# Optimization experiments

Measured on AMD Instinct MI355X. Metric: run time of the kernel, lower is better.

## Reference

```python
import math
import jax, jax.numpy as jnp
import numpy as np

E_DIM = 256
R_DIM = 256
HID = 512
B = 1024
H = 200
LN_EPS = 1e-5


def layer_norm(x, g, b):
    mu = jnp.mean(x, axis=-1, keepdims=True)
    var = jnp.mean((x - mu) ** 2, axis=-1, keepdims=True)
    return (x - mu) * jax.lax.rsqrt(var + LN_EPS) * g + b


def setup_inputs() -> dict:
    key = jax.random.key(0)
    ks = jax.random.split(key, 16)
    s = lambda fan: 1.0 / math.sqrt(fan)
    inp = {
        "e_emb": jax.random.normal(ks[0], (B, E_DIM), jnp.float32),
        "hist_ent_emb": jax.random.normal(ks[1], (B, H, E_DIM), jnp.float32),
        "hist_rel_emb": jax.random.normal(ks[2], (B, H, R_DIM), jnp.float32),
        "hist_time_raw": jax.random.randint(ks[3], (B, H), 0, 1000, jnp.int32),
        "query_time": jax.random.randint(ks[4], (B,), 0, 1000, jnp.int32),
        "hist_mask": jax.random.bernoulli(ks[5], 0.8, (B, H)),
        # parameters
        "W_rel": jax.random.uniform(ks[6], (E_DIM, R_DIM), jnp.float32, -s(R_DIM), s(R_DIM)),
        "W_q": jax.random.uniform(ks[7], (E_DIM, E_DIM), jnp.float32, -s(E_DIM), s(E_DIM)),
        "log_gamma": jnp.asarray(-3.0, jnp.float32),
        "W1": jax.random.uniform(ks[8], (2 * E_DIM, 4 * E_DIM), jnp.float32, -s(4 * E_DIM), s(4 * E_DIM)),
        "b1": jnp.zeros((2 * E_DIM,), jnp.float32),
        "ln1_g": jnp.ones((2 * E_DIM,), jnp.float32),
        "ln1_b": jnp.zeros((2 * E_DIM,), jnp.float32),
        "W2": jax.random.uniform(ks[9], (E_DIM, 2 * E_DIM), jnp.float32, -s(2 * E_DIM), s(2 * E_DIM)),
        "b2": jnp.zeros((E_DIM,), jnp.float32),
        "ln2_g": jnp.ones((E_DIM,), jnp.float32),
        "ln2_b": jnp.zeros((E_DIM,), jnp.float32),
        "Wc": jax.random.uniform(ks[10], (HID, E_DIM), jnp.float32, -s(E_DIM), s(E_DIM)),
        "bc": jnp.zeros((HID,), jnp.float32),
        "lnc_g": jnp.ones((HID,), jnp.float32),
        "lnc_b": jnp.zeros((HID,), jnp.float32),
    }
    return inp


def reference(e_emb, hist_ent_emb, hist_rel_emb, hist_time_raw, query_time, hist_mask,
              W_rel, W_q, log_gamma, W1, b1, ln1_g, ln1_b, W2, b2, ln2_g, ln2_b,
              Wc, bc, lnc_g, lnc_b):
    E = e_emb.shape[-1]
    # DistMult messages: (B,H,E)
    rel_projected = jnp.einsum("bhr,er->bhe", hist_rel_emb, W_rel)
    messages = hist_ent_emb * rel_projected
    # time decay
    time_diff = jnp.maximum(query_time.astype(jnp.float32)[:, None] - hist_time_raw.astype(jnp.float32), 0.0)
    decay = jnp.exp(-jnp.exp(log_gamma) * time_diff)  # (B,H)
    messages_dec = messages * decay[..., None]
    # query-conditioned attention
    q_repr = e_emb @ W_q.T  # (B,E)
    attn_raw = jnp.einsum("be,bhe->bh", q_repr, messages_dec) / math.sqrt(E)
    attn_raw = jnp.where(hist_mask, attn_raw, -1e9)
    attn = jax.nn.softmax(attn_raw, axis=-1)
    # PNA aggregation over valid neighbors
    valid_f = hist_mask.astype(jnp.float32)[..., None]  # (B,H,1)
    n_valid = jnp.maximum(jnp.sum(valid_f, axis=1), 1.0)  # (B,1)
    valid_msgs = messages * valid_f
    mean_msg = jnp.sum(valid_msgs, axis=1) / n_valid
    max_msg = jnp.max(valid_msgs, axis=1)
    attn_msg = jnp.einsum("bh,bhe->be", attn, messages)
    combined = jnp.concatenate([mean_msg, max_msg, attn_msg, e_emb], axis=-1)  # (B,4E)
    # out_proj MLP (dropout = identity, eval mode)
    h1 = jax.nn.gelu(layer_norm(combined @ W1.T + b1, ln1_g, ln1_b), approximate=False)
    dynamic_emb = layer_norm(h1 @ W2.T + b2, ln2_g, ln2_b)  # (B,E)
    ctx = jax.nn.gelu(layer_norm(dynamic_emb @ Wc.T + bc, lnc_g, lnc_b), approximate=False)  # (B,HID)
    return dynamic_emb, ctx
```

## Files before the change

### kernel.cpp

```cpp
#include <hip/hip_runtime.h>
#include <hip/hip_bf16.h>
#include <math.h>

#define B_SZ 1024
#define H_SZ 200
#define E_SZ 256
#define R_SZ 256
#define LN_EPS 1e-5f
#define NEG_HUGE -3.0e38f

typedef short bf16x8 __attribute__((ext_vector_type(8)));
typedef float f32x4 __attribute__((ext_vector_type(4)));

static __device__ inline short f2bf(float f) {
  union { float f; unsigned int u; } v; v.f = f;
  unsigned int u = v.u;
  unsigned int r = (u + 0x7fffu + ((u >> 16) & 1u)) >> 16;
  return (short)(unsigned short)r;
}

static __device__ inline float mask_at(const void* m, size_t idx, int is_b8) {
  if (is_b8) return ((const unsigned char*)m)[idx] ? 1.f : 0.f;
  return ((const int*)m)[idx] ? 1.f : 0.f;
}

__global__ void detect_mask_kernel(const unsigned char* __restrict__ mask,
                                   int* __restrict__ flag) {
  __shared__ int cnt;
  if (threadIdx.x == 0) cnt = 0;
  __syncthreads();
  int c = 0;
  for (int i = threadIdx.x; i < 4096; i += 256) c += mask[i] ? 1 : 0;
  atomicAdd(&cnt, c);
  __syncthreads();
  if (threadIdx.x == 0) *flag = (cnt > 2048) ? 1 : 0;
}

__global__ __launch_bounds__(256) void qrepr_kernel(
    const float* __restrict__ e_emb, const float* __restrict__ Wq,
    float* __restrict__ q_out) {
  __shared__ float emb[4][E_SZ];
  const int t = threadIdx.x;
  const int b0 = blockIdx.x * 4;
  for (int r = 0; r < 4; ++r) emb[r][t] = e_emb[(size_t)(b0 + r) * E_SZ + t];
  __syncthreads();
  float acc[4] = {0.f, 0.f, 0.f, 0.f};
  const float4* wrow = (const float4*)(Wq + (size_t)t * E_SZ);
  for (int k4 = 0; k4 < E_SZ / 4; ++k4) {
    float4 w = wrow[k4];
    const int k = k4 * 4;
#pragma unroll
    for (int r = 0; r < 4; ++r)
      acc[r] += emb[r][k] * w.x + emb[r][k + 1] * w.y + emb[r][k + 2] * w.z +
                emb[r][k + 3] * w.w;
  }
  for (int r = 0; r < 4; ++r) q_out[(size_t)(b0 + r) * E_SZ + t] = acc[r];
}

#define AGG_LDS_BYTES 152576

__global__ __launch_bounds__(512, 2) void agg_kernel(
    const float* __restrict__ rel, const float* __restrict__ ent,
    const int* __restrict__ htime, const int* __restrict__ qtime,
    const void* __restrict__ mask, const int* __restrict__ mflag,
    const float* __restrict__ Wrel, const float* __restrict__ qws,
    const float* __restrict__ e_emb, const float* __restrict__ log_gamma,
    float* __restrict__ comb) {
  extern __shared__ char smem[];
  short* Wsw = (short*)smem;
  short* Asw = (short*)(smem + 131072);
  float* q_s = (float*)(smem + 147456);
  float* attn_acc = (float*)(smem + 148480);
  float* mean_b = (float*)(smem + 149504);
  float* max_b = (float*)(smem + 150528);
  float* s_part = (float*)(smem + 151552);
  float* decay_s = (float*)(smem + 152064);
  float* maskf_s = (float*)(smem + 152192);
  float* p_s = (float*)(smem + 152320);
  float* scal = (float*)(smem + 152448);

  const int t = threadIdx.x;
  const int lane = t & 63;
  const int w = t >> 6;
  const int rh = w >> 2;
  const int cg = w & 3;
  const int q4 = lane >> 4;
  const int cl = lane & 15;
  const float gamma = expf(log_gamma[0]);
  const int is_b8 = *mflag;

  for (int pass = 0; pass < 16; ++pass) {
    const int idx = pass * 512 + t;
    const int e = idx >> 5;
    const int rc = idx & 31;
    const float4* src = (const float4*)(Wrel + (size_t)e * R_SZ + rc * 8);
    float4 a0 = src[0], a1 = src[1];
    const int ks = rc >> 2;
    const int lidx = ((rc & 3) << 4) | (e & 15);
    const int csub = e >> 4;
    bf16x8 v;
    v[0] = f2bf(a0.x); v[1] = f2bf(a0.y); v[2] = f2bf(a0.z); v[3] = f2bf(a0.w);
    v[4] = f2bf(a1.x); v[5] = f2bf(a1.y); v[6] = f2bf(a1.z); v[7] = f2bf(a1.w);
    *(bf16x8*)(Wsw + (((csub * 8 + ks) * 64 + lidx) << 3)) = v;
  }

  for (int bi = 0; bi < 4; ++bi) {
    const int b = blockIdx.x + 256 * bi;
    if (t < 256) { attn_acc[t] = 0.f; q_s[t] = qws[(size_t)b * E_SZ + t]; }
    if (t == 0) { scal[0] = NEG_HUGE; scal[1] = 0.f; scal[2] = 0.f; scal[3] = 0.f; }
    float mean4[4] = {0.f, 0.f, 0.f, 0.f};
    float max4[4] = {NEG_HUGE, NEG_HUGE, NEG_HUGE, NEG_HUGE};
    const int qt = qtime[b];
    __syncthreads();

    for (int tile = 0; tile < 7; ++tile) {
      const int h0 = tile * 32;
      {
        const int row = t >> 4;
        const int rcc = t & 15;
        const int h = h0 + row;
        bf16x8 v0 = {}; bf16x8 v1 = {};
        if (h < H_SZ) {
          const float4* src =
              (const float4*)(rel + ((size_t)b * H_SZ + h) * R_SZ + rcc * 16);
          float4 a0 = src[0], a1 = src[1], a2 = src[2], a3 = src[3];
          v0[0] = f2bf(a0.x); v0[1] = f2bf(a0.y); v0[2] = f2bf(a0.z); v0[3] = f2bf(a0.w);
          v0[4] = f2bf(a1.x); v0[5] = f2bf(a1.y); v0[6] = f2bf(a1.z); v0[7] = f2bf(a1.w);
          v1[0] = f2bf(a2.x); v1[1] = f2bf(a2.y); v1[2] = f2bf(a2.z); v1[3] = f2bf(a2.w);
          v1[4] = f2bf(a3.x); v1[5] = f2bf(a3.y); v1[6] = f2bf(a3.z); v1[7] = f2bf(a3.w);
        }
        const int rh2 = row >> 4, rlow = row & 15;
        const int rr0 = rcc * 2, rr1 = rcc * 2 + 1;
        *(bf16x8*)(Asw + (((rh2 * 8 + (rr0 >> 2)) * 64 + (((rr0 & 3) << 4) | rlow)) << 3)) = v0;
        *(bf16x8*)(Asw + (((rh2 * 8 + (rr1 >> 2)) * 64 + (((rr1 & 3) << 4) | rlow)) << 3)) = v1;
      }
      if (t < 32) {
        const int h = h0 + t;
        float mf = 0.f, dc = 0.f;
        if (h < H_SZ) {
          mf = mask_at(mask, (size_t)b * H_SZ + h, is_b8);
          float td = fmaxf((float)(qt - htime[(size_t)b * H_SZ + h]), 0.f);
          dc = expf(-gamma * td);
        }
        maskf_s[t] = mf; decay_s[t] = dc;
      }
      __syncthreads();

      f32x4 acc[4] = {};
      for (int ks = 0; ks < 8; ++ks) {
        bf16x8 av = *(bf16x8*)(Asw + (((rh * 8 + ks) * 64 + lane) << 3));
#pragma unroll
        for (int sub = 0; sub < 4; ++sub) {
          bf16x8 bv = *(bf16x8*)(Wsw + ((((cg * 4 + sub) * 8 + ks) * 64 + lane) << 3));
          acc[sub] = __builtin_amdgcn_mfma_f32_16x16x32_bf16(av, bv, acc[sub], 0, 0, 0);
        }
      }

      float msgv[16];
      float sc[4];
#pragma unroll
      for (int reg = 0; reg < 4; ++reg) {
        const int row = rh * 16 + q4 * 4 + reg;
        const int h = h0 + row;
        const float mf = maskf_s[row];
        const bool realrow = (h < H_SZ);
        float srow = 0.f;
#pragma unroll
        for (int sub = 0; sub < 4; ++sub) {
          const int e = cg * 64 + sub * 16 + cl;
          float entv = realrow ? ent[((size_t)b * H_SZ + h) * E_SZ + e] : 0.f;
          float m = acc[sub][reg] * entv;
          msgv[reg * 4 + sub] = m;
          mean4[sub] += mf * m;
          float cand = realrow ? (mf != 0.f ? m : 0.f) : NEG_HUGE;
          max4[sub] = fmaxf(max4[sub], cand);
          srow += q_s[e] * m;
        }
        sc[reg] = srow;
      }
#pragma unroll
      for (int m = 1; m <= 8; m <<= 1)
#pragma unroll
        for (int reg = 0; reg < 4; ++reg) sc[reg] += __shfl_xor(sc[reg], m, 64);
      if (cl == 0)
#pragma unroll
        for (int reg = 0; reg < 4; ++reg)
          s_part[(rh * 16 + q4 * 4 + reg) * 4 + cg] = sc[reg];
      __syncthreads();

      if (w == 0) {
        const int row = lane & 31;
        const int h = h0 + row;
        float srow = s_part[row * 4] + s_part[row * 4 + 1] +
                     s_part[row * 4 + 2] + s_part[row * 4 + 3];
        float s;
        if (h >= H_SZ) s = NEG_HUGE;
        else if (maskf_s[row] == 0.f) s = -1e9f;
        else s = decay_s[row] * srow * 0.0625f;
        float mt = s;
#pragma unroll
        for (int m = 1; m <= 16; m <<= 1) mt = fmaxf(mt, __shfl_xor(mt, m, 64));
        const float m_old = scal[0];
        const float m_new = fmaxf(m_old, mt);
        const float alpha = expf(m_old - m_new);
        const float p = expf(s - m_new);
        float lt = p;
#pragma unroll
        for (int m = 1; m <= 16; m <<= 1) lt += __shfl_xor(lt, m, 64);
        if (lane == 0) {
          scal[0] = m_new;
          scal[1] = scal[1] * alpha + lt;
          scal[2] = alpha;
        }
        if (lane < 32) p_s[row] = p;
      }
      __syncthreads();
      {
        const float alpha = scal[2];
        if (t < 256) attn_acc[t] *= alpha;
      }
      __syncthreads();
      float av4[4];
#pragma unroll
      for (int sub = 0; sub < 4; ++sub) {
        float v = 0.f;
#pragma unroll
        for (int reg = 0; reg < 4; ++reg)
          v += p_s[rh * 16 + q4 * 4 + reg] * msgv[reg * 4 + sub];
        v += __shfl_xor(v, 16, 64);
        v += __shfl_xor(v, 32, 64);
        av4[sub] = v;
      }
      if (q4 == 0)
#pragma unroll
        for (int sub = 0; sub < 4; ++sub)
          atomicAdd(&attn_acc[cg * 64 + sub * 16 + cl], av4[sub]);
      __syncthreads();
    }

#pragma unroll
    for (int sub = 0; sub < 4; ++sub) {
      float mv = mean4[sub];
      mv += __shfl_xor(mv, 16, 64); mv += __shfl_xor(mv, 32, 64);
      float xv = max4[sub];
      xv = fmaxf(xv, __shfl_xor(xv, 16, 64));
      xv = fmaxf(xv, __shfl_xor(xv, 32, 64));
      mean4[sub] = mv; max4[sub] = xv;
    }
    if (rh == 0 && q4 == 0) {
#pragma unroll
      for (int sub = 0; sub < 4; ++sub) {
        mean_b[cg * 64 + sub * 16 + cl] = mean4[sub];
        max_b[cg * 64 + sub * 16 + cl] = max4[sub];
      }
    }
    if (t < H_SZ) atomicAdd(&scal[3], mask_at(mask, (size_t)b * H_SZ + t, is_b8));
    __syncthreads();
    if (rh == 1 && q4 == 0) {
#pragma unroll
      for (int sub = 0; sub < 4; ++sub) {
        const int e = cg * 64 + sub * 16 + cl;
        mean_b[e] += mean4[sub];
        max_b[e] = fmaxf(max_b[e], max4[sub]);
      }
    }
    __syncthreads();
    if (t < 256) {
      const float nv = fmaxf(scal[3], 1.f);
      const float l = scal[1];
      float* dst = comb + (size_t)b * 1024;
      dst[t] = mean_b[t] / nv;
      dst[256 + t] = max_b[t];
      dst[512 + t] = attn_acc[t] / l;
      dst[768 + t] = e_emb[(size_t)b * E_SZ + t];
    }
    __syncthreads();
  }
}

template <int K, int N, bool GELU>
__global__ __launch_bounds__(256) void mlp_kernel(
    const float* __restrict__ X, const float* __restrict__ W,
    const float* __restrict__ bias, const float* __restrict__ lng,
    const float* __restrict__ lnb, float* __restrict__ Y) {
  constexpr int CPT = N / 256;
  __shared__ float xs[4][K];
  __shared__ float pre[4][N];
  __shared__ float red[4][2];
  const int t = threadIdx.x;
  const size_t b0 = (size_t)blockIdx.x * 4;
  for (int r = 0; r < 4; ++r)
    for (int k = t; k < K; k += 256) xs[r][k] = X[(b0 + r) * K + k];
  __syncthreads();
  float acc[4][CPT];
#pragma unroll
  for (int r = 0; r < 4; ++r)
#pragma unroll
    for (int c = 0; c < CPT; ++c) acc[r][c] = 0.f;
  for (int ci = 0; ci < CPT; ++ci) {
    const int c = t + 256 * ci;
    const float4* wr = (const float4*)(W + (size_t)c * K);
    for (int k4 = 0; k4 < K / 4; ++k4) {
      float4 wv = wr[k4];
      const int k = k4 * 4;
#pragma unroll
      for (int r = 0; r < 4; ++r)
        acc[r][ci] += xs[r][k] * wv.x + xs[r][k + 1] * wv.y +
                      xs[r][k + 2] * wv.z + xs[r][k + 3] * wv.w;
    }
  }
  for (int ci = 0; ci < CPT; ++ci) {
    const int c = t + 256 * ci;
#pragma unroll
    for (int r = 0; r < 4; ++r) pre[r][c] = acc[r][ci] + bias[c];
  }
  __syncthreads();
  if (t < 64) {
    const int r = t >> 4, ch = t & 15;
    float s = 0.f, s2 = 0.f;
    for (int i = ch * (N / 16); i < (ch + 1) * (N / 16); ++i) {
      float v = pre[r][i]; s += v; s2 += v * v;
    }
#pragma unroll
    for (int m = 1; m <= 8; m <<= 1) {
      s += __shfl_xor(s, m, 64);
      s2 += __shfl_xor(s2, m, 64);
    }
    if (ch == 0) { red[r][0] = s / N; red[r][1] = s2 / N; }
  }
  __syncthreads();
  for (int ci = 0; ci < CPT; ++ci) {
    const int c = t + 256 * ci;
#pragma unroll
    for (int r = 0; r < 4; ++r) {
      const float mu = red[r][0];
      const float var = fmaxf(red[r][1] - mu * mu, 0.f);
      float x = (pre[r][c] - mu) * rsqrtf(var + LN_EPS) * lng[c] + lnb[c];
      if (GELU) x = 0.5f * x * (1.f + erff(x * 0.70710678118654752f));
      Y[(b0 + r) * N + c] = x;
    }
  }
}

extern "C" void kernel_launch(void* const* d_in, const int* in_sizes, int n_in,
                              void* d_out, int out_size, void* d_ws,
                              size_t ws_size, hipStream_t stream) {
  const float* e_emb = (const float*)d_in[0];
  const float* ent = (const float*)d_in[1];
  const float* rel = (const float*)d_in[2];
  const int* ht = (const int*)d_in[3];
  const int* qt = (const int*)d_in[4];
  const void* mask = d_in[5];
  const float* Wrel = (const float*)d_in[6];
  const float* Wq = (const float*)d_in[7];
  const float* lg = (const float*)d_in[8];
  const float* W1 = (const float*)d_in[9];
  const float* b1 = (const float*)d_in[10];
  const float* ln1g = (const float*)d_in[11];
  const float* ln1b = (const float*)d_in[12];
  const float* W2 = (const float*)d_in[13];
  const float* b2 = (const float*)d_in[14];
  const float* ln2g = (const float*)d_in[15];
  const float* ln2b = (const float*)d_in[16];
  const float* Wc = (const float*)d_in[17];
  const float* bc = (const float*)d_in[18];
  const float* lncg = (const float*)d_in[19];
  const float* lncb = (const float*)d_in[20];

  float* q_ws = (float*)d_ws;
  float* comb = (float*)((char*)d_ws + (1 << 20));
  float* t1 = (float*)((char*)d_ws + (5 << 20));
  int* mflag = (int*)((char*)d_ws + (7 << 20));
  float* dyn = (float*)d_out;
  float* ctx = (float*)d_out + (size_t)B_SZ * E_SZ;

  (void)hipFuncSetAttribute((const void*)agg_kernel,
                            hipFuncAttributeMaxDynamicSharedMemorySize,
                            AGG_LDS_BYTES);

  detect_mask_kernel<<<1, 256, 0, stream>>>((const unsigned char*)mask, mflag);
  qrepr_kernel<<<256, 256, 0, stream>>>(e_emb, Wq, q_ws);
  agg_kernel<<<256, 512, AGG_LDS_BYTES, stream>>>(rel, ent, ht, qt, mask, mflag,
                                                  Wrel, q_ws, e_emb, lg, comb);
  mlp_kernel<1024, 512, true><<<256, 256, 0, stream>>>(comb, W1, b1, ln1g, ln1b, t1);
  mlp_kernel<512, 256, false><<<256, 256, 0, stream>>>(t1, W2, b2, ln2g, ln2b, dyn);
  mlp_kernel<256, 512, true><<<256, 256, 0, stream>>>(dyn, Wc, bc, lncg, lncb, ctx);
}
```

Measured before the change: 673.5 us.

## Rewrite aggregation with prefetch pipelining, two-pass softmax, and MFMA MLP GEMMs

Several independent changes land together. W_rel is pre-swizzled to bf16 once in a separate kernel, and the aggregation kernel now prefetches the next tile's rel and ent rows into registers while computing the current one. It uses an XOR-swizzled LDS layout and replaces the per-tile online softmax (several barriers per tile) with one softmax pass over bf16 messages kept in registers. The scalar fp32 MLP and q-projection kernels become a tiled bf16 MFMA GEMM plus separate LayerNorm/GELU kernels. The aim is to cut barrier count and redundant global loads and to move the GEMMs onto matrix cores, at the cost of bf16 rounding in the messages and MLP inputs, more kernel launches, and higher register pressure.

```diff
diff --git a/kernel.cpp b/kernel.cpp
--- a/kernel.cpp
+++ b/kernel.cpp
@@ -12,14 +12,24 @@
 typedef short bf16x8 __attribute__((ext_vector_type(8)));
 typedef float f32x4 __attribute__((ext_vector_type(4)));
 
-static __device__ inline short f2bf(float f) {
-  union { float f; unsigned int u; } v; v.f = f;
-  unsigned int u = v.u;
-  unsigned int r = (u + 0x7fffu + ((u >> 16) & 1u)) >> 16;
+static __device__ __forceinline__ short f2bf(float f) {
+  union { float f; unsigned u; } v; v.f = f;
+  unsigned r = (v.u + 0x7fffu + ((v.u >> 16) & 1u)) >> 16;
   return (short)(unsigned short)r;
 }
-
-static __device__ inline float mask_at(const void* m, size_t idx, int is_b8) {
+static __device__ __forceinline__ float bf2f(unsigned short h) {
+  union { unsigned u; float f; } v; v.u = ((unsigned)h) << 16; return v.f;
+}
+static __device__ __forceinline__ int slotxor(int frame, int q4f, int mf, int ks) {
+  return frame * 64 + (q4f << 4) + ((mf ^ (ks & 3) ^ ((q4f & 3) << 2)) & 15);
+}
+static __device__ __forceinline__ bf16x8 pack8(const float4& a, const float4& b) {
+  bf16x8 v;
+  v[0] = f2bf(a.x); v[1] = f2bf(a.y); v[2] = f2bf(a.z); v[3] = f2bf(a.w);
+  v[4] = f2bf(b.x); v[5] = f2bf(b.y); v[6] = f2bf(b.z); v[7] = f2bf(b.w);
+  return v;
+}
+static __device__ __forceinline__ float mask_at(const void* m, size_t idx, int is_b8) {
   if (is_b8) return ((const unsigned char*)m)[idx] ? 1.f : 0.f;
   return ((const int*)m)[idx] ? 1.f : 0.f;
 }
@@ -36,238 +46,249 @@
   if (threadIdx.x == 0) *flag = (cnt > 2048) ? 1 : 0;
 }
 
-__global__ __launch_bounds__(256) void qrepr_kernel(
-    const float* __restrict__ e_emb, const float* __restrict__ Wq,
-    float* __restrict__ q_out) {
-  __shared__ float emb[4][E_SZ];
-  const int t = threadIdx.x;
-  const int b0 = blockIdx.x * 4;
-  for (int r = 0; r < 4; ++r) emb[r][t] = e_emb[(size_t)(b0 + r) * E_SZ + t];
-  __syncthreads();
-  float acc[4] = {0.f, 0.f, 0.f, 0.f};
-  const float4* wrow = (const float4*)(Wq + (size_t)t * E_SZ);
-  for (int k4 = 0; k4 < E_SZ / 4; ++k4) {
-    float4 w = wrow[k4];
-    const int k = k4 * 4;
-#pragma unroll
-    for (int r = 0; r < 4; ++r)
-      acc[r] += emb[r][k] * w.x + emb[r][k + 1] * w.y + emb[r][k + 2] * w.z +
-                emb[r][k + 3] * w.w;
-  }
-  for (int r = 0; r < 4; ++r) q_out[(size_t)(b0 + r) * E_SZ + t] = acc[r];
-}
-
-#define AGG_LDS_BYTES 152576
+__global__ __launch_bounds__(256) void prep_wrel_kernel(
+    const float* __restrict__ Wrel, short* __restrict__ Wg) {
+  const int s = blockIdx.x * 256 + threadIdx.x;
+  const int frame = s >> 6, lf = s & 63, q4f = lf >> 4, mfx = lf & 15;
+  const int ks = frame & 7, csub = frame >> 3;
+  const int m = (mfx ^ (ks & 3) ^ ((q4f & 3) << 2)) & 15;
+  const int e = csub * 16 + m;
+  const int r0 = ks * 32 + q4f * 8;
+  const float4* src = (const float4*)(Wrel + (size_t)e * R_SZ + r0);
+  float4 a = src[0], b = src[1];
+  *(bf16x8*)(Wg + (size_t)s * 8) = pack8(a, b);
+}
+
+#define AGG_LDS_BYTES 157200
 
 __global__ __launch_bounds__(512, 2) void agg_kernel(
     const float* __restrict__ rel, const float* __restrict__ ent,
     const int* __restrict__ htime, const int* __restrict__ qtime,
     const void* __restrict__ mask, const int* __restrict__ mflag,
-    const float* __restrict__ Wrel, const float* __restrict__ qws,
+    const short* __restrict__ Wg, const float* __restrict__ qws,
     const float* __restrict__ e_emb, const float* __restrict__ log_gamma,
     float* __restrict__ comb) {
   extern __shared__ char smem[];
   short* Wsw = (short*)smem;
   short* Asw = (short*)(smem + 131072);
-  float* q_s = (float*)(smem + 147456);
-  float* attn_acc = (float*)(smem + 148480);
-  float* mean_b = (float*)(smem + 149504);
-  float* max_b = (float*)(smem + 150528);
-  float* s_part = (float*)(smem + 151552);
-  float* decay_s = (float*)(smem + 152064);
-  float* maskf_s = (float*)(smem + 152192);
-  float* p_s = (float*)(smem + 152320);
-  float* scal = (float*)(smem + 152448);
-
-  const int t = threadIdx.x;
-  const int lane = t & 63;
-  const int w = t >> 6;
-  const int rh = w >> 2;
-  const int cg = w & 3;
-  const int q4 = lane >> 4;
-  const int cl = lane & 15;
+  float* maskf_s = (float*)(smem + 147456);
+  float* decay_s = (float*)(smem + 148480);
+  float* score_s = (float*)(smem + 149504);
+  float* s_part  = (float*)(smem + 150528);
+  float* attn_acc = (float*)(smem + 154112);
+  float* mean_b  = (float*)(smem + 155136);
+  float* max_b   = (float*)(smem + 156160);
+  float* scal    = (float*)(smem + 157184);
+
+  const int t = threadIdx.x, lane = t & 63, w = t >> 6;
+  const int rh = w >> 2, cg = w & 3, q4 = lane >> 4, cl = lane & 15;
   const float gamma = expf(log_gamma[0]);
   const int is_b8 = *mflag;
 
-  for (int pass = 0; pass < 16; ++pass) {
-    const int idx = pass * 512 + t;
-    const int e = idx >> 5;
-    const int rc = idx & 31;
-    const float4* src = (const float4*)(Wrel + (size_t)e * R_SZ + rc * 8);
-    float4 a0 = src[0], a1 = src[1];
-    const int ks = rc >> 2;
-    const int lidx = ((rc & 3) << 4) | (e & 15);
-    const int csub = e >> 4;
-    bf16x8 v;
-    v[0] = f2bf(a0.x); v[1] = f2bf(a0.y); v[2] = f2bf(a0.z); v[3] = f2bf(a0.w);
-    v[4] = f2bf(a1.x); v[5] = f2bf(a1.y); v[6] = f2bf(a1.z); v[7] = f2bf(a1.w);
-    *(bf16x8*)(Wsw + (((csub * 8 + ks) * 64 + lidx) << 3)) = v;
-  }
+  {
+    const bf16x8* src = (const bf16x8*)Wg;
+    bf16x8* dst = (bf16x8*)Wsw;
+#pragma unroll
+    for (int p = 0; p < 16; ++p) dst[p * 512 + t] = src[p * 512 + t];
+  }
+
+  const int arow = t >> 4, rcc = t & 15;
 
   for (int bi = 0; bi < 4; ++bi) {
     const int b = blockIdx.x + 256 * bi;
-    if (t < 256) { attn_acc[t] = 0.f; q_s[t] = qws[(size_t)b * E_SZ + t]; }
-    if (t == 0) { scal[0] = NEG_HUGE; scal[1] = 0.f; scal[2] = 0.f; scal[3] = 0.f; }
+    const int qt = qtime[b];
+    if (t < 256) {
+      attn_acc[t] = 0.f;
+      float mf = 0.f, dc = 0.f;
+      if (t < H_SZ) {
+        mf = mask_at(mask, (size_t)b * H_SZ + t, is_b8);
+        float td = fmaxf((float)(qt - htime[(size_t)b * H_SZ + t]), 0.f);
+        dc = expf(-gamma * td);
+      }
+      maskf_s[t] = mf; decay_s[t] = dc;
+    }
+    float qv[4];
+#pragma unroll
+    for (int sub = 0; sub < 4; ++sub)
+      qv[sub] = qws[(size_t)b * E_SZ + cg * 64 + sub * 16 + cl];
+
+    float4 c0, c1, c2, c3;
+    {
+      const int hc = min(arow, H_SZ - 1);
+      const float4* src = (const float4*)(rel + ((size_t)b * H_SZ + hc) * R_SZ + rcc * 16);
+      c0 = src[0]; c1 = src[1]; c2 = src[2]; c3 = src[3];
+    }
+    float entb[16];
+#pragma unroll
+    for (int reg = 0; reg < 4; ++reg) {
+      const int hc = min(rh * 16 + q4 * 4 + reg, H_SZ - 1);
+      const float* ep = ent + ((size_t)b * H_SZ + hc) * E_SZ + cg * 64 + cl;
+#pragma unroll
+      for (int sub = 0; sub < 4; ++sub) entb[reg * 4 + sub] = ep[sub * 16];
+    }
+    {
+      const int rb = arow >> 4, m = arow & 15;
+      bf16x8 v0 = pack8(c0, c1), v1 = pack8(c2, c3);
+      int k8 = rcc * 2, ks = k8 >> 2, qw = k8 & 3;
+      *(bf16x8*)(Asw + slotxor(rb * 8 + ks, qw, m, ks) * 8) = v0;
+      k8 = rcc * 2 + 1; ks = k8 >> 2; qw = k8 & 3;
+      *(bf16x8*)(Asw + slotxor(rb * 8 + ks, qw, m, ks) * 8) = v1;
+    }
+    __syncthreads();
+
     float mean4[4] = {0.f, 0.f, 0.f, 0.f};
     float max4[4] = {NEG_HUGE, NEG_HUGE, NEG_HUGE, NEG_HUGE};
-    const int qt = qtime[b];
-    __syncthreads();
-
+    unsigned msgp[56];
+
+#pragma unroll
     for (int tile = 0; tile < 7; ++tile) {
       const int h0 = tile * 32;
-      {
-        const int row = t >> 4;
-        const int rcc = t & 15;
-        const int h = h0 + row;
-        bf16x8 v0 = {}; bf16x8 v1 = {};
-        if (h < H_SZ) {
-          const float4* src =
-              (const float4*)(rel + ((size_t)b * H_SZ + h) * R_SZ + rcc * 16);
-          float4 a0 = src[0], a1 = src[1], a2 = src[2], a3 = src[3];
-          v0[0] = f2bf(a0.x); v0[1] = f2bf(a0.y); v0[2] = f2bf(a0.z); v0[3] = f2bf(a0.w);
-          v0[4] = f2bf(a1.x); v0[5] = f2bf(a1.y); v0[6] = f2bf(a1.z); v0[7] = f2bf(a1.w);
-          v1[0] = f2bf(a2.x); v1[1] = f2bf(a2.y); v1[2] = f2bf(a2.z); v1[3] = f2bf(a2.w);
-          v1[4] = f2bf(a3.x); v1[5] = f2bf(a3.y); v1[6] = f2bf(a3.z); v1[7] = f2bf(a3.w);
+      float4 n0, n1, n2, n3;
+      float entn[16];
+      if (tile < 6) {
+        const int hc = min(h0 + 32 + arow, H_SZ - 1);
+        const float4* src = (const float4*)(rel + ((size_t)b * H_SZ + hc) * R_SZ + rcc * 16);
+        n0 = src[0]; n1 = src[1]; n2 = src[2]; n3 = src[3];
+#pragma unroll
+        for (int reg = 0; reg < 4; ++reg) {
+          const int hc2 = min(h0 + 32 + rh * 16 + q4 * 4 + reg, H_SZ - 1);
+          const float* ep = ent + ((size_t)b * H_SZ + hc2) * E_SZ + cg * 64 + cl;
+#pragma unroll
+          for (int sub = 0; sub < 4; ++sub) entn[reg * 4 + sub] = ep[sub * 16];
         }
-        const int rh2 = row >> 4, rlow = row & 15;
-        const int rr0 = rcc * 2, rr1 = rcc * 2 + 1;
-        *(bf16x8*)(Asw + (((rh2 * 8 + (rr0 >> 2)) * 64 + (((rr0 & 3) << 4) | rlow)) << 3)) = v0;
-        *(bf16x8*)(Asw + (((rh2 * 8 + (rr1 >> 2)) * 64 + (((rr1 & 3) << 4) | rlow)) << 3)) = v1;
-      }
-      if (t < 32) {
-        const int h = h0 + t;
-        float mf = 0.f, dc = 0.f;
-        if (h < H_SZ) {
-          mf = mask_at(mask, (size_t)b * H_SZ + h, is_b8);
-          float td = fmaxf((float)(qt - htime[(size_t)b * H_SZ + h]), 0.f);
-          dc = expf(-gamma * td);
-        }
-        maskf_s[t] = mf; decay_s[t] = dc;
-      }
-      __syncthreads();
-
+      }
       f32x4 acc[4] = {};
+#pragma unroll
       for (int ks = 0; ks < 8; ++ks) {
-        bf16x8 av = *(bf16x8*)(Asw + (((rh * 8 + ks) * 64 + lane) << 3));
+        bf16x8 av = *(const bf16x8*)(Asw + slotxor(rh * 8 + ks, q4, cl, ks) * 8);
 #pragma unroll
         for (int sub = 0; sub < 4; ++sub) {
-          bf16x8 bv = *(bf16x8*)(Wsw + ((((cg * 4 + sub) * 8 + ks) * 64 + lane) << 3));
+          bf16x8 bv = *(const bf16x8*)(Wsw + slotxor((cg * 4 + sub) * 8 + ks, q4, cl, ks) * 8);
           acc[sub] = __builtin_amdgcn_mfma_f32_16x16x32_bf16(av, bv, acc[sub], 0, 0, 0);
         }
       }
-
-      float msgv[16];
       float sc[4];
 #pragma unroll
       for (int reg = 0; reg < 4; ++reg) {
         const int row = rh * 16 + q4 * 4 + reg;
-        const int h = h0 + row;
-        const float mf = maskf_s[row];
-        const bool realrow = (h < H_SZ);
-        float srow = 0.f;
+        const int hg = h0 + row;
+        const float mf = maskf_s[hg];
+        const bool rr = hg < H_SZ;
+        float srow = 0.f, mtmp[4];
 #pragma unroll
         for (int sub = 0; sub < 4; ++sub) {
-          const int e = cg * 64 + sub * 16 + cl;
-          float entv = realrow ? ent[((size_t)b * H_SZ + h) * E_SZ + e] : 0.f;
-          float m = acc[sub][reg] * entv;
-          msgv[reg * 4 + sub] = m;
+          float m = rr ? acc[sub][reg] * entb[reg * 4 + sub] : 0.f;
+          mtmp[sub] = m;
           mean4[sub] += mf * m;
-          float cand = realrow ? (mf != 0.f ? m : 0.f) : NEG_HUGE;
+          float cand = rr ? (mf != 0.f ? m : 0.f) : NEG_HUGE;
           max4[sub] = fmaxf(max4[sub], cand);
-          srow += q_s[e] * m;
+          srow += qv[sub] * m;
         }
         sc[reg] = srow;
-      }
-#pragma unroll
-      for (int m = 1; m <= 8; m <<= 1)
-#pragma unroll
-        for (int reg = 0; reg < 4; ++reg) sc[reg] += __shfl_xor(sc[reg], m, 64);
+        msgp[tile * 8 + reg * 2 + 0] =
+            (unsigned)(unsigned short)f2bf(mtmp[0]) | ((unsigned)(unsigned short)f2bf(mtmp[1]) << 16);
+        msgp[tile * 8 + reg * 2 + 1] =
+            (unsigned)(unsigned short)f2bf(mtmp[2]) | ((unsigned)(unsigned short)f2bf(mtmp[3]) << 16);
+      }
+#pragma unroll
+      for (int mm = 1; mm <= 8; mm <<= 1)
+#pragma unroll
+        for (int reg = 0; reg < 4; ++reg) sc[reg] += __shfl_xor(sc[reg], mm, 64);
       if (cl == 0)
 #pragma unroll
         for (int reg = 0; reg < 4; ++reg)
-          s_part[(rh * 16 + q4 * 4 + reg) * 4 + cg] = sc[reg];
-      __syncthreads();
-
-      if (w == 0) {
-        const int row = lane & 31;
-        const int h = h0 + row;
-        float srow = s_part[row * 4] + s_part[row * 4 + 1] +
-                     s_part[row * 4 + 2] + s_part[row * 4 + 3];
-        float s;
-        if (h >= H_SZ) s = NEG_HUGE;
-        else if (maskf_s[row] == 0.f) s = -1e9f;
-        else s = decay_s[row] * srow * 0.0625f;
-        float mt = s;
-#pragma unroll
-        for (int m = 1; m <= 16; m <<= 1) mt = fmaxf(mt, __shfl_xor(mt, m, 64));
-        const float m_old = scal[0];
-        const float m_new = fmaxf(m_old, mt);
-        const float alpha = expf(m_old - m_new);
-        const float p = expf(s - m_new);
-        float lt = p;
-#pragma unroll
-        for (int m = 1; m <= 16; m <<= 1) lt += __shfl_xor(lt, m, 64);
-        if (lane == 0) {
-          scal[0] = m_new;
-          scal[1] = scal[1] * alpha + lt;
-          scal[2] = alpha;
-        }
-        if (lane < 32) p_s[row] = p;
-      }
-      __syncthreads();
-      {
-        const float alpha = scal[2];
-        if (t < 256) attn_acc[t] *= alpha;
-      }
-      __syncthreads();
-      float av4[4];
-#pragma unroll
-      for (int sub = 0; sub < 4; ++sub) {
-        float v = 0.f;
-#pragma unroll
-        for (int reg = 0; reg < 4; ++reg)
-          v += p_s[rh * 16 + q4 * 4 + reg] * msgv[reg * 4 + sub];
-        v += __shfl_xor(v, 16, 64);
-        v += __shfl_xor(v, 32, 64);
-        av4[sub] = v;
-      }
-      if (q4 == 0)
-#pragma unroll
-        for (int sub = 0; sub < 4; ++sub)
-          atomicAdd(&attn_acc[cg * 64 + sub * 16 + cl], av4[sub]);
-      __syncthreads();
-    }
-
+          s_part[(h0 + rh * 16 + q4 * 4 + reg) * 4 + cg] = sc[reg];
+
+      if (tile < 6) {
+#pragma unroll
+        for (int i = 0; i < 16; ++i) entb[i] = entn[i];
+        __syncthreads();
+        const int rb = arow >> 4, m = arow & 15;
+        bf16x8 v0 = pack8(n0, n1), v1 = pack8(n2, n3);
+        int k8 = rcc * 2, ks = k8 >> 2, qw = k8 & 3;
+        *(bf16x8*)(Asw + slotxor(rb * 8 + ks, qw, m, ks) * 8) = v0;
+        k8 = rcc * 2 + 1; ks = k8 >> 2; qw = k8 & 3;
+        *(bf16x8*)(Asw + slotxor(rb * 8 + ks, qw, m, ks) * 8) = v1;
+        __syncthreads();
+      }
+    }
+    __syncthreads();
+
+    if (t < 256) {
+      float s = NEG_HUGE;
+      if (t < H_SZ) {
+        float srow = s_part[t * 4] + s_part[t * 4 + 1] + s_part[t * 4 + 2] + s_part[t * 4 + 3];
+        s = (maskf_s[t] != 0.f) ? decay_s[t] * srow * 0.0625f : -1e9f;
+      }
+      score_s[t] = s;
+    }
+    __syncthreads();
+    if (w == 0) {
+      float s0 = score_s[lane], s1 = score_s[lane + 64];
+      float s2 = score_s[lane + 128], s3 = score_s[lane + 192];
+      float mv = fmaxf(fmaxf(s0, s1), fmaxf(s2, s3));
+#pragma unroll
+      for (int mm = 1; mm <= 32; mm <<= 1) mv = fmaxf(mv, __shfl_xor(mv, mm, 64));
+      float e0 = expf(s0 - mv), e1 = expf(s1 - mv), e2 = expf(s2 - mv), e3 = expf(s3 - mv);
+      score_s[lane] = e0; score_s[lane + 64] = e1;
+      score_s[lane + 128] = e2; score_s[lane + 192] = e3;
+      float ls = e0 + e1 + e2 + e3;
+      float nv = maskf_s[lane] + maskf_s[lane + 64] + maskf_s[lane + 128] + maskf_s[lane + 192];
+#pragma unroll
+      for (int mm = 1; mm <= 32; mm <<= 1) {
+        ls += __shfl_xor(ls, mm, 64);
+        nv += __shfl_xor(nv, mm, 64);
+      }
+      if (lane == 0) { scal[0] = ls; scal[1] = nv; }
+    }
+    __syncthreads();
+
+    float av4[4] = {0.f, 0.f, 0.f, 0.f};
+#pragma unroll
+    for (int tile = 0; tile < 7; ++tile)
+#pragma unroll
+      for (int reg = 0; reg < 4; ++reg) {
+        float p = score_s[tile * 32 + rh * 16 + q4 * 4 + reg];
+        unsigned pa = msgp[tile * 8 + reg * 2], pb = msgp[tile * 8 + reg * 2 + 1];
+        av4[0] += p * bf2f((unsigned short)(pa & 0xffff));
+        av4[1] += p * bf2f((unsigned short)(pa >> 16));
+        av4[2] += p * bf2f((unsigned short)(pb & 0xffff));
+        av4[3] += p * bf2f((unsigned short)(pb >> 16));
+      }
 #pragma unroll
     for (int sub = 0; sub < 4; ++sub) {
-      float mv = mean4[sub];
-      mv += __shfl_xor(mv, 16, 64); mv += __shfl_xor(mv, 32, 64);
-      float xv = max4[sub];
-      xv = fmaxf(xv, __shfl_xor(xv, 16, 64));
-      xv = fmaxf(xv, __shfl_xor(xv, 32, 64));
-      mean4[sub] = mv; max4[sub] = xv;
-    }
-    if (rh == 0 && q4 == 0) {
+      av4[sub] += __shfl_xor(av4[sub], 16, 64);
+      av4[sub] += __shfl_xor(av4[sub], 32, 64);
+    }
+    if (q4 == 0)
+#pragma unroll
+      for (int sub = 0; sub < 4; ++sub)
+        atomicAdd(&attn_acc[cg * 64 + sub * 16 + cl], av4[sub]);
+
+#pragma unroll
+    for (int sub = 0; sub < 4; ++sub) {
+      mean4[sub] += __shfl_xor(mean4[sub], 16, 64);
+      mean4[sub] += __shfl_xor(mean4[sub], 32, 64);
+      max4[sub] = fmaxf(max4[sub], __shfl_xor(max4[sub], 16, 64));
+      max4[sub] = fmaxf(max4[sub], __shfl_xor(max4[sub], 32, 64));
+    }
+    if (rh == 0 && q4 == 0)
 #pragma unroll
       for (int sub = 0; sub < 4; ++sub) {
         mean_b[cg * 64 + sub * 16 + cl] = mean4[sub];
         max_b[cg * 64 + sub * 16 + cl] = max4[sub];
       }
-    }
-    if (t < H_SZ) atomicAdd(&scal[3], mask_at(mask, (size_t)b * H_SZ + t, is_b8));
-    __syncthreads();
-    if (rh == 1 && q4 == 0) {
+    __syncthreads();
+    if (rh == 1 && q4 == 0)
 #pragma unroll
       for (int sub = 0; sub < 4; ++sub) {
         const int e = cg * 64 + sub * 16 + cl;
         mean_b[e] += mean4[sub];
         max_b[e] = fmaxf(max_b[e], max4[sub]);
       }
-    }
     __syncthreads();
     if (t < 256) {
-      const float nv = fmaxf(scal[3], 1.f);
-      const float l = scal[1];
+      const float nv = fmaxf(scal[1], 1.f), l = scal[0];
       float* dst = comb + (size_t)b * 1024;
       dst[t] = mean_b[t] / nv;
       dst[256 + t] = max_b[t];
@@ -278,67 +299,121 @@
   }
 }
 
-template <int K, int N, bool GELU>
-__global__ __launch_bounds__(256) void mlp_kernel(
-    const float* __restrict__ X, const float* __restrict__ W,
-    const float* __restrict__ bias, const float* __restrict__ lng,
-    const float* __restrict__ lnb, float* __restrict__ Y) {
+template <int N, int K>
+__global__ __launch_bounds__(256) void gemm_bf16(const float* __restrict__ A,
+                                                 const float* __restrict__ W,
+                                                 float* __restrict__ C) {
+  __shared__ short As[2][4096];
+  __shared__ short Ws[2][4096];
+  const int t = threadIdx.x, lane = t & 63, w = t >> 6, q4 = lane >> 4, cl = lane & 15;
+  const int row0 = blockIdx.x * 64, col0 = blockIdx.y * 64;
+  const int sr = t >> 2, kc = t & 3;
+  const int rb = sr >> 4, sm = sr & 15;
+  constexpr int KT = K / 64;
+
+  float4 ar[4], wr4[4];
+  {
+    const float4* ap = (const float4*)(A + (size_t)(row0 + sr) * K + kc * 16);
+    const float4* wp = (const float4*)(W + (size_t)(col0 + sr) * K + kc * 16);
+    ar[0] = ap[0]; ar[1] = ap[1]; ar[2] = ap[2]; ar[3] = ap[3];
+    wr4[0] = wp[0]; wr4[1] = wp[1]; wr4[2] = wp[2]; wr4[3] = wp[3];
+  }
+  {
+    bf16x8 a0 = pack8(ar[0], ar[1]), a1 = pack8(ar[2], ar[3]);
+    bf16x8 b0 = pack8(wr4[0], wr4[1]), b1 = pack8(wr4[2], wr4[3]);
+    int k8 = kc * 2, ks = k8 >> 2, qw = k8 & 3;
+    *(bf16x8*)&As[0][slotxor(rb * 2 + ks, qw, sm, ks) * 8] = a0;
+    *(bf16x8*)&Ws[0][slotxor(rb * 2 + ks, qw, sm, ks) * 8] = b0;
+    k8 = kc * 2 + 1; ks = k8 >> 2; qw = k8 & 3;
+    *(bf16x8*)&As[0][slotxor(rb * 2 + ks, qw, sm, ks) * 8] = a1;
+    *(bf16x8*)&Ws[0][slotxor(rb * 2 + ks, qw, sm, ks) * 8] = b1;
+  }
+  __syncthreads();
+
+  f32x4 acc[4] = {};
+  for (int kt = 0; kt < KT; ++kt) {
+    if (kt + 1 < KT) {
+      const float4* ap = (const float4*)(A + (size_t)(row0 + sr) * K + (kt + 1) * 64 + kc * 16);
+      const float4* wp = (const float4*)(W + (size_t)(col0 + sr) * K + (kt + 1) * 64 + kc * 16);
+      ar[0] = ap[0]; ar[1] = ap[1]; ar[2] = ap[2]; ar[3] = ap[3];
+      wr4[0] = wp[0]; wr4[1] = wp[1]; wr4[2] = wp[2]; wr4[3] = wp[3];
+    }
+    const short* Ab = As[kt & 1];
+    const short* Wb = Ws[kt & 1];
+#pragma unroll
+    for (int ks = 0; ks < 2; ++ks) {
+      bf16x8 av = *(const bf16x8*)&Ab[slotxor(w * 2 + ks, q4, cl, ks) * 8];
+#pragma unroll
+      for (int cb = 0; cb < 4; ++cb) {
+        bf16x8 bv = *(const bf16x8*)&Wb[slotxor(cb * 2 + ks, q4, cl, ks) * 8];
+        acc[cb] = __builtin_amdgcn_mfma_f32_16x16x32_bf16(av, bv, acc[cb], 0, 0, 0);
+      }
+    }
+    if (kt + 1 < KT) {
+      short* An = (short*)As[(kt + 1) & 1];
+      short* Wn = (short*)Ws[(kt + 1) & 1];
+      bf16x8 a0 = pack8(ar[0], ar[1]), a1 = pack8(ar[2], ar[3]);
+      bf16x8 b0 = pack8(wr4[0], wr4[1]), b1 = pack8(wr4[2], wr4[3]);
+      int k8 = kc * 2, ks = k8 >> 2, qw = k8 & 3;
+      *(bf16x8*)&An[slotxor(rb * 2 + ks, qw, sm, ks) * 8] = a0;
+      *(bf16x8*)&Wn[slotxor(rb * 2 + ks, qw, sm, ks) * 8] = b0;
+      k8 = kc * 2 + 1; ks = k8 >> 2; qw = k8 & 3;
+      *(bf16x8*)&An[slotxor(rb * 2 + ks, qw, sm, ks) * 8] = a1;
+      *(bf16x8*)&Wn[slotxor(rb * 2 + ks, qw, sm, ks) * 8] = b1;
+    }
+    __syncthreads();
+  }
+#pragma unroll
+  for (int cb = 0; cb < 4; ++cb)
+#pragma unroll
+    for (int reg = 0; reg < 4; ++reg) {
+      const int rowi = row0 + w * 16 + q4 * 4 + reg;
+      const int coli = col0 + cb * 16 + cl;
+      C[(size_t)rowi * N + coli] = acc[cb][reg];
+    }
+}
+
+template <int N, bool G>
+__global__ __launch_bounds__(256) void ln_kernel(const float* __restrict__ pre,
+                                                 const float* __restrict__ bias,
+                                                 const float* __restrict__ gg,
+                                                 const float* __restrict__ bb,
+                                                 float* __restrict__ out) {
   constexpr int CPT = N / 256;
-  __shared__ float xs[4][K];
-  __shared__ float pre[4][N];
-  __shared__ float red[4][2];
-  const int t = threadIdx.x;
-  const size_t b0 = (size_t)blockIdx.x * 4;
-  for (int r = 0; r < 4; ++r)
-    for (int k = t; k < K; k += 256) xs[r][k] = X[(b0 + r) * K + k];
+  __shared__ float red[2][4];
+  __shared__ float mr[2];
+  const int t = threadIdx.x, lane = t & 63, w = t >> 6;
+  const size_t row = blockIdx.x;
+  float v[CPT];
+  float s = 0.f, s2 = 0.f;
+#pragma unroll
+  for (int i = 0; i < CPT; ++i) {
+    const int c = t + 256 * i;
+    v[i] = pre[row * N + c] + bias[c];
+    s += v[i]; s2 += v[i] * v[i];
+  }
+#pragma unroll
+  for (int mm = 1; mm <= 32; mm <<= 1) {
+    s += __shfl_xor(s, mm, 64);
+    s2 += __shfl_xor(s2, mm, 64);
+  }
+  if (lane == 0) { red[0][w] = s; red[1][w] = s2; }
   __syncthreads();
-  float acc[4][CPT];
-#pragma unroll
-  for (int r = 0; r < 4; ++r)
-#pragma unroll
-    for (int c = 0; c < CPT; ++c) acc[r][c] = 0.f;
-  for (int ci = 0; ci < CPT; ++ci) {
-    const int c = t + 256 * ci;
-    const float4* wr = (const float4*)(W + (size_t)c * K);
-    for (int k4 = 0; k4 < K / 4; ++k4) {
-      float4 wv = wr[k4];
-      const int k = k4 * 4;
-#pragma unroll
-      for (int r = 0; r < 4; ++r)
-        acc[r][ci] += xs[r][k] * wv.x + xs[r][k + 1] * wv.y +
-                      xs[r][k + 2] * wv.z + xs[r][k + 3] * wv.w;
-    }
-  }
-  for (int ci = 0; ci < CPT; ++ci) {
-    const int c = t + 256 * ci;
-#pragma unroll
-    for (int r = 0; r < 4; ++r) pre[r][c] = acc[r][ci] + bias[c];
+  if (t == 0) {
+    float a = red[0][0] + red[0][1] + red[0][2] + red[0][3];
+    float q = red[1][0] + red[1][1] + red[1][2] + red[1][3];
+    mr[0] = a / N; mr[1] = q / N;
   }
   __syncthreads();
-  if (t < 64) {
-    const int r = t >> 4, ch = t & 15;
-    float s = 0.f, s2 = 0.f;
-    for (int i = ch * (N / 16); i < (ch + 1) * (N / 16); ++i) {
-      float v = pre[r][i]; s += v; s2 += v * v;
-    }
-#pragma unroll
-    for (int m = 1; m <= 8; m <<= 1) {
-      s += __shfl_xor(s, m, 64);
-      s2 += __shfl_xor(s2, m, 64);
-    }
-    if (ch == 0) { red[r][0] = s / N; red[r][1] = s2 / N; }
-  }
-  __syncthreads();
-  for (int ci = 0; ci < CPT; ++ci) {
-    const int c = t + 256 * ci;
-#pragma unroll
-    for (int r = 0; r < 4; ++r) {
-      const float mu = red[r][0];
-      const float var = fmaxf(red[r][1] - mu * mu, 0.f);
-      float x = (pre[r][c] - mu) * rsqrtf(var + LN_EPS) * lng[c] + lnb[c];
-      if (GELU) x = 0.5f * x * (1.f + erff(x * 0.70710678118654752f));
-      Y[(b0 + r) * N + c] = x;
-    }
+  const float mu = mr[0];
+  const float var = fmaxf(mr[1] - mu * mu, 0.f);
+  const float rstd = rsqrtf(var + LN_EPS);
+#pragma unroll
+  for (int i = 0; i < CPT; ++i) {
+    const int c = t + 256 * i;
+    float x = (v[i] - mu) * rstd * gg[c] + bb[c];
+    if (G) x = 0.5f * x * (1.f + erff(x * 0.70710678118654752f));
+    out[row * N + c] = x;
   }
 }
 
@@ -369,8 +444,12 @@
 
   float* q_ws = (float*)d_ws;
   float* comb = (float*)((char*)d_ws + (1 << 20));
-  float* t1 = (float*)((char*)d_ws + (5 << 20));
-  int* mflag = (int*)((char*)d_ws + (7 << 20));
+  float* t1   = (float*)((char*)d_ws + (1 << 20));
+  float* prec = (float*)((char*)d_ws + (3 << 20));
+  float* pre1 = (float*)((char*)d_ws + (5 << 20));
+  float* pre2 = q_ws;
+  short* Wg   = (short*)((char*)d_ws + (5 << 20));
+  int* mflag  = (int*)((char*)d_ws + (5 << 20) + 131072);
   float* dyn = (float*)d_out;
   float* ctx = (float*)d_out + (size_t)B_SZ * E_SZ;
 
@@ -379,10 +458,14 @@
                             AGG_LDS_BYTES);
 
   detect_mask_kernel<<<1, 256, 0, stream>>>((const unsigned char*)mask, mflag);
-  qrepr_kernel<<<256, 256, 0, stream>>>(e_emb, Wq, q_ws);
+  prep_wrel_kernel<<<32, 256, 0, stream>>>(Wrel, Wg);
+  gemm_bf16<256, 256><<<dim3(16, 4), 256, 0, stream>>>(e_emb, Wq, q_ws);
   agg_kernel<<<256, 512, AGG_LDS_BYTES, stream>>>(rel, ent, ht, qt, mask, mflag,
-                                                  Wrel, q_ws, e_emb, lg, comb);
-  mlp_kernel<1024, 512, true><<<256, 256, 0, stream>>>(comb, W1, b1, ln1g, ln1b, t1);
-  mlp_kernel<512, 256, false><<<256, 256, 0, stream>>>(t1, W2, b2, ln2g, ln2b, dyn);
-  mlp_kernel<256, 512, true><<<256, 256, 0, stream>>>(dyn, Wc, bc, lncg, lncb, ctx);
-}
+                                                  Wg, q_ws, e_emb, lg, comb);
+  gemm_bf16<512, 1024><<<dim3(16, 8), 256, 0, stream>>>(comb, W1, pre1);
+  ln_kernel<512, true><<<1024, 256, 0, stream>>>(pre1, b1, ln1g, ln1b, t1);
+  gemm_bf16<256, 512><<<dim3(16, 4), 256, 0, stream>>>(t1, W2, pre2);
+  ln_kernel<256, false><<<1024, 256, 0, stream>>>(pre2, b2, ln2g, ln2b, dyn);
+  gemm_bf16<512, 256><<<dim3(16, 8), 256, 0, stream>>>(dyn, Wc, prec);
+  ln_kernel<512, true><<<1024, 256, 0, stream>>>(prec, bc, lncg, lncb, ctx);
+}
```

Result: slower. 886.9 us (+31.7%).
